# Optimization experiments

Measured on AMD Instinct MI355X. Metric: run time of the kernel, lower is better.

## Reference

```python
import jax, jax.numpy as jnp
import numpy as np
from jax import lax

B = 8192          # batched independent VAD frames (original module is batch=1 streaming)
CUTOFF = 129      # STFT_CUTOFF
STRIDE = 128      # STFT_STRIDE
NFFT = 256        # STFT kernel length (inferred: pad 576->640, stride 128 -> 4 frames)
H = 128           # LSTM hidden size


def conv1d(x, w, b=None, stride=1, padding=0):
    # x: [B, Cin, T], w: [Cout, Cin, K]
    y = lax.conv_general_dilated(x, w, (stride,), [(padding, padding)],
                                 dimension_numbers=("NCH", "OIH", "NCH"))
    if b is not None:
        y = y + b[None, :, None]
    return y


def setup_inputs() -> dict:
    key = jax.random.key(0)
    ks = jax.random.split(key, 40)
    f32 = jnp.float32

    def rn(i, shape, scale=0.1):
        return jax.random.normal(ks[i], shape, dtype=f32) * scale

    inp = {
        "audio": jax.random.normal(ks[0], (B, 576), dtype=f32),
        "h": jnp.zeros((B, H), dtype=f32),
        "c": jnp.zeros((B, H), dtype=f32),
        # STFT basis: 129 real + 129 imag cosine/sine rows, kernel 256
        "forward_basis": rn(1, (2 * CUTOFF, 1, NFFT), 0.1),
        # encoder: 4 conv1d+relu blocks (Silero v5 layout)
        "enc_w1": rn(2, (128, 129, 3)), "enc_b1": rn(3, (128,)),
        "enc_w2": rn(4, (64, 128, 3)), "enc_b2": rn(5, (64,)),
        "enc_w3": rn(6, (64, 64, 3)),  "enc_b3": rn(7, (64,)),
        "enc_w4": rn(8, (128, 64, 3)), "enc_b4": rn(9, (128,)),
        # LSTM cell weights
        "wi": rn(10, (H, H)), "wf": rn(11, (H, H)), "wg": rn(12, (H, H)), "wo": rn(13, (H, H)),
        "ui": rn(14, (H, H)), "uf": rn(15, (H, H)), "ug": rn(16, (H, H)), "uo": rn(17, (H, H)),
        "bxi": rn(18, (H,)), "bxf": rn(19, (H,)), "bxg": rn(20, (H,)), "bxo": rn(21, (H,)),
        "bhi": rn(22, (H,)), "bhf": rn(23, (H,)), "bhg": rn(24, (H,)), "bho": rn(25, (H,)),
        # output head: conv1d 128 -> 1, kernel 1
        "conv_w": rn(26, (1, H, 1)), "conv_b": rn(27, (1,)),
    }
    return inp


def reference(audio, h, c, forward_basis,
              enc_w1, enc_b1, enc_w2, enc_b2, enc_w3, enc_b3, enc_w4, enc_b4,
              wi, wf, wg, wo, ui, uf, ug, uo,
              bxi, bxf, bxg, bxo, bhi, bhf, bhg, bho,
              conv_w, conv_b):
    # STFT via strided conv1d on reflect-padded audio
    x = jnp.pad(audio, ((0, 0), (0, 64)), mode="reflect")[:, None, :]   # [B,1,640]
    x = conv1d(x, forward_basis, stride=STRIDE)                          # [B,258,4]
    real, imag = x[:, :CUTOFF, :], x[:, CUTOFF:, :]
    mag = jnp.sqrt(real ** 2 + imag ** 2)                                # [B,129,4]

    # encoder: conv+relu stack, T: 4 -> 4 -> 2 -> 1 -> 1
    e = jax.nn.relu(conv1d(mag, enc_w1, enc_b1, stride=1, padding=1))
    e = jax.nn.relu(conv1d(e, enc_w2, enc_b2, stride=2, padding=1))
    e = jax.nn.relu(conv1d(e, enc_w3, enc_b3, stride=2, padding=1))
    e = jax.nn.relu(conv1d(e, enc_w4, enc_b4, stride=1, padding=1))
    x = e[:, :, 0]                                                       # [B,128]

    lin = lambda v, W, b: v @ W.T + b
    i_gate = jax.nn.sigmoid(lin(x, wi, bxi) + lin(h, ui, bhi))
    f_gate = jax.nn.sigmoid(lin(x, wf, bxf) + lin(h, uf, bhf))
    g_gate = jnp.tanh(lin(x, wg, bxg) + lin(h, ug, bhg))
    o_gate = jax.nn.sigmoid(lin(x, wo, bxo) + lin(h, uo, bho))
    c_out = f_gate * c + i_gate * g_gate
    h_out = o_gate * jnp.tanh(c_out)

    # output head: relu -> conv1d(128->1, k=1) -> sigmoid -> mean over T(=1)
    y = jax.nn.relu(h_out)                                               # [B,128]
    logit = y @ conv_w[0, :, 0] + conv_b[0]                              # [B]
    prob = jax.nn.sigmoid(logit)[:, None]                                # [B,1]
    return prob, h_out, c_out
```

## Files before the change

### kernel.cpp

```cpp
#include <hip/hip_runtime.h>
#include <math.h>

#define BATCH 8192
typedef unsigned short u16;
typedef unsigned int u32;
typedef __attribute__((ext_vector_type(8))) short bf16x8;
typedef __attribute__((ext_vector_type(4))) float f32x4;
typedef __attribute__((ext_vector_type(4))) unsigned short u16x4;

__device__ __forceinline__ float sigm(float v) { return 1.0f / (1.0f + __expf(-v)); }
__device__ __forceinline__ u16 f2bf(float f) {
    union { float f; u32 u; } v; v.f = f;
    u32 r = v.u + 0x7FFFu + ((v.u >> 16) & 1u);
    return (u16)(r >> 16);
}
__device__ __forceinline__ float bf2f(u16 h) {
    union { u32 u; float f; } v; v.u = ((u32)h) << 16; return v.f;
}
__device__ __forceinline__ void split_store4(float4 v, u16* hp, u16* lp) {
    u16 h0 = f2bf(v.x), h1 = f2bf(v.y), h2 = f2bf(v.z), h3 = f2bf(v.w);
    u16x4 hv = {h0, h1, h2, h3};
    u16x4 lv = {f2bf(v.x - bf2f(h0)), f2bf(v.y - bf2f(h1)),
                f2bf(v.z - bf2f(h2)), f2bf(v.w - bf2f(h3))};
    *(u16x4*)hp = hv; *(u16x4*)lp = lv;
}
__device__ __forceinline__ bf16x8 bfrag(const u16* Bf, int nt, int ch, int nch, int lane) {
    return *(const bf16x8*)(Bf + (((size_t)nt * nch + ch) * 64 + lane) * 8);
}
#define MFMA(a, b, c) __builtin_amdgcn_mfma_f32_16x16x32_bf16(a, b, c, 0, 0, 0)

#define S_FBT 69632
#define S_B1  61440
#define S_B2A 16384
#define S_B2B 24576
#define S_B3  8192
#define S_B4  8192
#define S_BL  131072
#define P_FBT 0
#define P_B1  139264
#define P_B2A 262144
#define P_B2B 294912
#define P_B3  344064
#define P_B4  360448
#define P_BL  376832
#define WEND  638976
#define N_PREP 319488

__global__ __launch_bounds__(256) void k_prep(const float* __restrict__ fb,
                                              const float* __restrict__ w1, const float* __restrict__ w2,
                                              const float* __restrict__ w3, const float* __restrict__ w4,
                                              const float* __restrict__ wi, const float* __restrict__ wf,
                                              const float* __restrict__ wg, const float* __restrict__ wo,
                                              const float* __restrict__ ui, const float* __restrict__ uf,
                                              const float* __restrict__ ug, const float* __restrict__ uo,
                                              u16* __restrict__ wsu) {
    const float* Ws[8] = {wi, wf, wg, wo, ui, uf, ug, uo};
    for (int i = blockIdx.x * 256 + threadIdx.x; i < N_PREP; i += gridDim.x * 256) {
        int r = i;
        float v; int P, S, idx;
        if (r < S_FBT) {
            int f = r >> 9, lane = (r & 511) >> 3, e = r & 7;
            int n = (f >> 3) * 16 + (lane & 15), k = (f & 7) * 32 + (lane >> 4) * 8 + e;
            int c = n >> 1, part = n & 1;
            v = (n < 258) ? fb[(size_t)(c + part * 129) * 256 + k] : 0.f;
            P = P_FBT; S = S_FBT; idx = r;
        } else if ((r -= S_FBT) < S_B1) {
            int kk = r / 20480, r2 = r - kk * 20480;
            int f = r2 >> 9, lane = (r2 & 511) >> 3, e = r2 & 7;
            int n = (f / 5) * 16 + (lane & 15), k = (f % 5) * 32 + (lane >> 4) * 8 + e;
            v = (k < 129) ? w1[(size_t)n * 387 + k * 3 + kk] : 0.f;
            P = P_B1; S = S_B1; idx = r;
        } else if ((r -= S_B1) < S_B2A) {
            int f = r >> 9, lane = (r & 511) >> 3, e = r & 7;
            int n = (f >> 3) * 16 + (lane & 15), k = (f & 7) * 32 + (lane >> 4) * 8 + e;
            v = w2[(size_t)n * 384 + (k & 127) * 3 + (k >> 7) + 1];
            P = P_B2A; S = S_B2A; idx = r;
        } else if ((r -= S_B2A) < S_B2B) {
            int f = r >> 9, lane = (r & 511) >> 3, e = r & 7;
            int n = (f / 12) * 16 + (lane & 15), k = (f % 12) * 32 + (lane >> 4) * 8 + e;
            v = w2[(size_t)n * 384 + (k & 127) * 3 + (k >> 7)];
            P = P_B2B; S = S_B2B; idx = r;
        } else if ((r -= S_B2B) < S_B3) {
            int f = r >> 9, lane = (r & 511) >> 3, e = r & 7;
            int n = (f >> 2) * 16 + (lane & 15), k = (f & 3) * 32 + (lane >> 4) * 8 + e;
            v = w3[(size_t)n * 192 + (k & 63) * 3 + (k >> 6) + 1];
            P = P_B3; S = S_B3; idx = r;
        } else if ((r -= S_B3) < S_B4) {
            int f = r >> 9, lane = (r & 511) >> 3, e = r & 7;
            int n = (f >> 1) * 16 + (lane & 15), k = (f & 1) * 32 + (lane >> 4) * 8 + e;
            v = w4[(size_t)n * 192 + k * 3 + 1];
            P = P_B4; S = S_B4; idx = r;
        } else {
            r -= S_B4;
            int f = r >> 9, lane = (r & 511) >> 3, e = r & 7;
            int n = (f >> 3) * 16 + (lane & 15), k = (f & 7) * 32 + (lane >> 4) * 8 + e;
            int g = n >> 7, j = n & 127;
            v = Ws[g + ((k >= 128) ? 4 : 0)][(size_t)j * 128 + (k & 127)];
            P = P_BL; S = S_BL; idx = r;
        }
        u16 h = f2bf(v);
        wsu[P + idx] = h;
        wsu[P + S + idx] = f2bf(v - bf2f(h));
    }
}

__global__ __launch_bounds__(512) void k_fused1(const float* __restrict__ audio,
                                                const u16* __restrict__ wsu,
                                                const float* __restrict__ b1,
                                                u16* __restrict__ E1H, u16* __restrict__ E1L) {
    __shared__ __align__(16) u16 uni[32256];
    u16* aAh = uni;
    u16* aAl = uni + 11520;
    u16* mAh = uni;
    u16* mAl = uni + 16128;
    const int tid = threadIdx.x;
    const int b0 = blockIdx.x << 4;
    for (int i = tid; i < 16 * 160; i += 512) {
        int bb = i / 160, j4 = (i - bb * 160) * 4;
        const float* ap = audio + (size_t)(b0 + bb) * 576;
        float4 v;
        if (j4 < 576) v = *(const float4*)(ap + j4);
        else { v.x = ap[1150 - j4]; v.y = ap[1149 - j4]; v.z = ap[1148 - j4]; v.w = ap[1147 - j4]; }
        int phys = bb * 720 + j4 + (j4 >> 7) * 8;
        split_store4(v, aAh + phys, aAl + phys);
    }
    __syncthreads();
    const int lane = tid & 63, w = tid >> 6;
    const int m = lane & 15, quad = lane >> 4;
    const u16* fbT = wsu + P_FBT;
    const int tcnt = (w == 7) ? 3 : 2;
    f32x4 acc[4][3];
    #pragma unroll
    for (int mt = 0; mt < 4; ++mt)
        #pragma unroll
        for (int t = 0; t < 3; ++t) acc[mt][t] = (f32x4){0.f, 0.f, 0.f, 0.f};
    for (int ch = 0; ch < 8; ++ch) {
        bf16x8 ah[4], al[4];
        #pragma unroll
        for (int mt = 0; mt < 4; ++mt) {
            int Rm = mt * 16 + m;
            int phys = (Rm >> 2) * 720 + (Rm & 3) * 136 + ch * 32 + quad * 8 + ((ch >= 4) ? 8 : 0);
            ah[mt] = *(const bf16x8*)(aAh + phys);
            al[mt] = *(const bf16x8*)(aAl + phys);
        }
        #pragma unroll
        for (int tt = 0; tt < 3; ++tt) {
            if (tt < tcnt) {
                int t = w * 2 + tt;
                bf16x8 bh = bfrag(fbT, t, ch, 8, lane);
                bf16x8 bl_ = bfrag(fbT + S_FBT, t, ch, 8, lane);
                #pragma unroll
                for (int mt = 0; mt < 4; ++mt) {
                    acc[mt][tt] = MFMA(ah[mt], bh, acc[mt][tt]);
                    acc[mt][tt] = MFMA(ah[mt], bl_, acc[mt][tt]);
                    acc[mt][tt] = MFMA(al[mt], bh, acc[mt][tt]);
                }
            }
        }
    }
    __syncthreads();
    for (int i = tid; i < 16128; i += 512) ((u32*)uni)[i] = 0u;
    __syncthreads();
    #pragma unroll
    for (int tt = 0; tt < 3; ++tt) {
        if (tt < tcnt) {
            int n = (w * 2 + tt) * 16 + m;
            #pragma unroll
            for (int mt = 0; mt < 4; ++mt)
                #pragma unroll
                for (int r = 0; r < 4; ++r) {
                    float vv = acc[mt][tt][r];
                    float s = vv * vv;
                    s += __shfl_xor(s, 1);
                    if (!(n & 1)) {
                        int R = mt * 16 + quad * 4 + r;
                        int bb = R >> 2, t = R & 3, c = n >> 1;
                        float sv = sqrtf(s);
                        u16 h = f2bf(sv);
                        int phys = (bb * 6 + t + 1) * 168 + c;
                        mAh[phys] = h;
                        mAl[phys] = f2bf(sv - bf2f(h));
                    }
                }
        }
    }
    __syncthreads();
    const u16* B1h = wsu + P_B1;
    const u16* B1l = wsu + P_B1 + S_B1;
    f32x4 acc2[4];
    #pragma unroll
    for (int mt = 0; mt < 4; ++mt) acc2[mt] = (f32x4){0.f, 0.f, 0.f, 0.f};
    for (int kk = 0; kk < 3; ++kk) {
        for (int ch = 0; ch < 5; ++ch) {
            bf16x8 bh = bfrag(B1h + kk * 20480, w, ch, 5, lane);
            bf16x8 bl_ = bfrag(B1l + kk * 20480, w, ch, 5, lane);
            #pragma unroll
            for (int mt = 0; mt < 4; ++mt) {
                int Rm = mt * 16 + m;
                int phys = ((Rm >> 2) * 6 + (Rm & 3) + kk) * 168 + ch * 32 + quad * 8;
                bf16x8 ah = *(const bf16x8*)(mAh + phys);
                bf16x8 al = *(const bf16x8*)(mAl + phys);
                acc2[mt] = MFMA(ah, bh, acc2[mt]);
                acc2[mt] = MFMA(ah, bl_, acc2[mt]);
                acc2[mt] = MFMA(al, bh, acc2[mt]);
            }
        }
    }
    {
        int n = w * 16 + m;
        float bv = b1[n];
        #pragma unroll
        for (int mt = 0; mt < 4; ++mt)
            #pragma unroll
            for (int r = 0; r < 4; ++r) {
                int R = mt * 16 + quad * 4 + r;
                float vv = fmaxf(acc2[mt][r] + bv, 0.f);
                u16 h = f2bf(vv);
                size_t idx = (size_t)(b0 + (R >> 2)) * 512 + (R & 3) * 128 + n;
                E1H[idx] = h;
                E1L[idx] = f2bf(vv - bf2f(h));
            }
    }
}

__global__ __launch_bounds__(512) void k_fused2(const u16* __restrict__ E1H, const u16* __restrict__ E1L,
                                                const float* __restrict__ hin,
                                                const u16* __restrict__ wsu,
                                                const float* __restrict__ cin,
                                                const float* __restrict__ b2, const float* __restrict__ b3,
                                                const float* __restrict__ b4,
                                                const float* __restrict__ bxi, const float* __restrict__ bxf,
                                                const float* __restrict__ bxg, const float* __restrict__ bxo,
                                                const float* __restrict__ bhi, const float* __restrict__ bhf,
                                                const float* __restrict__ bhg, const float* __restrict__ bho,
                                                const float* __restrict__ cw, const float* __restrict__ cb,
                                                float* __restrict__ out) {
    __shared__ __align__(16) u16 eAh[16 * 520];
    __shared__ __align__(16) u16 eAl[16 * 520];
    __shared__ __align__(16) u16 s2h[16 * 136];
    __shared__ __align__(16) u16 s2l[16 * 136];
    __shared__ __align__(16) u16 s3h[16 * 72];
    __shared__ __align__(16) u16 s3l[16 * 72];
    __shared__ __align__(16) u16 xhh[16 * 264];
    __shared__ __align__(16) u16 xhl[16 * 264];
    __shared__ float pr[8][16];
    const int tid = threadIdx.x;
    const int b0 = blockIdx.x << 4;
    for (int i = tid; i < 16 * 64; i += 512) {
        int row = i >> 6, c8 = (i & 63) * 8;
        *(uint4*)(eAh + row * 520 + c8) = *(const uint4*)(E1H + (size_t)(b0 + row) * 512 + c8);
        *(uint4*)(eAl + row * 520 + c8) = *(const uint4*)(E1L + (size_t)(b0 + row) * 512 + c8);
    }
    for (int i = tid; i < 16 * 32; i += 512) {
        int row = i >> 5, c4 = (i & 31) * 4;
        float4 v = *(const float4*)(hin + (size_t)(b0 + row) * 128 + c4);
        split_store4(v, xhh + row * 264 + 128 + c4, xhl + row * 264 + 128 + c4);
    }
    __syncthreads();
    const int lane = tid & 63, w = tid >> 6;
    const int m = lane & 15, quad = lane >> 4;
    {
        const int isB = w >> 2, nt = w & 3;
        const int awoff = isB ? 128 : 0;
        const int nch = isB ? 12 : 8;
        const u16* Bh = wsu + (isB ? P_B2B : P_B2A);
        const u16* Bl = Bh + (isB ? S_B2B : S_B2A);
        f32x4 acc = (f32x4){0.f, 0.f, 0.f, 0.f};
        for (int ch = 0; ch < nch; ++ch) {
            int phys = m * 520 + awoff + ch * 32 + quad * 8;
            bf16x8 ah = *(const bf16x8*)(eAh + phys);
            bf16x8 al = *(const bf16x8*)(eAl + phys);
            bf16x8 bh = bfrag(Bh, nt, ch, nch, lane);
            bf16x8 bl_ = bfrag(Bl, nt, ch, nch, lane);
            acc = MFMA(ah, bh, acc);
            acc = MFMA(ah, bl_, acc);
            acc = MFMA(al, bh, acc);
        }
        const int oc = nt * 16 + m;
        const float bv = b2[oc];
        const int col = isB * 64 + oc;
        #pragma unroll
        for (int r = 0; r < 4; ++r) {
            int row = quad * 4 + r;
            float vv = fmaxf(acc[r] + bv, 0.f);
            u16 h = f2bf(vv);
            s2h[row * 136 + col] = h;
            s2l[row * 136 + col] = f2bf(vv - bf2f(h));
        }
    }
    __syncthreads();
    if (w < 4) {
        const u16* Bh = wsu + P_B3;
        const u16* Bl = Bh + S_B3;
        f32x4 acc = (f32x4){0.f, 0.f, 0.f, 0.f};
        for (int ch = 0; ch < 4; ++ch) {
            int phys = m * 136 + ch * 32 + quad * 8;
            bf16x8 ah = *(const bf16x8*)(s2h + phys);
            bf16x8 al = *(const bf16x8*)(s2l + phys);
            bf16x8 bh = bfrag(Bh, w, ch, 4, lane);
            bf16x8 bl_ = bfrag(Bl, w, ch, 4, lane);
            acc = MFMA(ah, bh, acc);
            acc = MFMA(ah, bl_, acc);
            acc = MFMA(al, bh, acc);
        }
        const int n = w * 16 + m;
        const float bv = b3[n];
        #pragma unroll
        for (int r = 0; r < 4; ++r) {
            int row = quad * 4 + r;
            float vv = fmaxf(acc[r] + bv, 0.f);
            u16 h = f2bf(vv);
            s3h[row * 72 + n] = h;
            s3l[row * 72 + n] = f2bf(vv - bf2f(h));
        }
    }
    __syncthreads();
    {
        const u16* Bh = wsu + P_B4;
        const u16* Bl = Bh + S_B4;
        f32x4 acc = (f32x4){0.f, 0.f, 0.f, 0.f};
        for (int ch = 0; ch < 2; ++ch) {
            int phys = m * 72 + ch * 32 + quad * 8;
            bf16x8 ah = *(const bf16x8*)(s3h + phys);
            bf16x8 al = *(const bf16x8*)(s3l + phys);
            bf16x8 bh = bfrag(Bh, w, ch, 2, lane);
            bf16x8 bl_ = bfrag(Bl, w, ch, 2, lane);
            acc = MFMA(ah, bh, acc);
            acc = MFMA(ah, bl_, acc);
            acc = MFMA(al, bh, acc);
        }
        const int n = w * 16 + m;
        const float bv = b4[n];
        #pragma unroll
        for (int r = 0; r < 4; ++r) {
            int row = quad * 4 + r;
            float vv = fmaxf(acc[r] + bv, 0.f);
            u16 h = f2bf(vv);
            xhh[row * 264 + n] = h;
            xhl[row * 264 + n] = f2bf(vv - bf2f(h));
        }
    }
    __syncthreads();
    {
        const u16* BLh = wsu + P_BL;
        const u16* BLl = BLh + S_BL;
        f32x4 acc[4];
        #pragma unroll
        for (int g = 0; g < 4; ++g) acc[g] = (f32x4){0.f, 0.f, 0.f, 0.f};
        for (int ch = 0; ch < 8; ++ch) {
            int phys = m * 264 + ch * 32 + quad * 8;
            bf16x8 ah = *(const bf16x8*)(xhh + phys);
            bf16x8 al = *(const bf16x8*)(xhl + phys);
            #pragma unroll
            for (int g = 0; g < 4; ++g) {
                int nt = g * 8 + w;
                bf16x8 bh = bfrag(BLh, nt, ch, 8, lane);
                bf16x8 bl_ = bfrag(BLl, nt, ch, 8, lane);
                acc[g] = MFMA(ah, bh, acc[g]);
                acc[g] = MFMA(ah, bl_, acc[g]);
                acc[g] = MFMA(al, bh, acc[g]);
            }
        }
        float partial[4];
        const int j = w * 16 + m;
        const float bi = bxi[j] + bhi[j];
        const float bff = bxf[j] + bhf[j];
        const float bgg = bxg[j] + bhg[j];
        const float boo = bxo[j] + bho[j];
        const float cwj = cw[j];
        #pragma unroll
        for (int r = 0; r < 4; ++r) {
            const int b = b0 + quad * 4 + r;
            const float ig = sigm(acc[0][r] + bi);
            const float fg = sigm(acc[1][r] + bff);
            const float gg = tanhf(acc[2][r] + bgg);
            const float og = sigm(acc[3][r] + boo);
            const float ci = cin[(size_t)b * 128 + j];
            const float co = fg * ci + ig * gg;
            const float ho = og * tanhf(co);
            out[(size_t)BATCH + (size_t)b * 128 + j] = ho;
            out[(size_t)BATCH + (size_t)BATCH * 128 + (size_t)b * 128 + j] = co;
            partial[r] = fmaxf(ho, 0.f) * cwj;
        }
        #pragma unroll
        for (int off = 1; off < 16; off <<= 1)
            #pragma unroll
            for (int r = 0; r < 4; ++r) partial[r] += __shfl_xor(partial[r], off);
        if (m == 0) {
            #pragma unroll
            for (int r = 0; r < 4; ++r) pr[w][quad * 4 + r] = partial[r];
        }
    }
    __syncthreads();
    if (tid < 16) {
        float s = cb[0];
        #pragma unroll
        for (int g = 0; g < 8; ++g) s += pr[g][tid];
        out[b0 + tid] = sigm(s);
    }
}

extern "C" void kernel_launch(void* const* d_in, const int* in_sizes, int n_in,
                              void* d_out, int out_size, void* d_ws, size_t ws_size,
                              hipStream_t stream) {
    const float* audio = (const float*)d_in[0];
    const float* hin   = (const float*)d_in[1];
    const float* cin   = (const float*)d_in[2];
    const float* fb    = (const float*)d_in[3];
    const float* w1    = (const float*)d_in[4];
    const float* b1    = (const float*)d_in[5];
    const float* w2    = (const float*)d_in[6];
    const float* b2    = (const float*)d_in[7];
    const float* w3    = (const float*)d_in[8];
    const float* b3    = (const float*)d_in[9];
    const float* w4    = (const float*)d_in[10];
    const float* b4    = (const float*)d_in[11];
    const float* wi    = (const float*)d_in[12];
    const float* wf    = (const float*)d_in[13];
    const float* wg    = (const float*)d_in[14];
    const float* wo    = (const float*)d_in[15];
    const float* ui    = (const float*)d_in[16];
    const float* uf    = (const float*)d_in[17];
    const float* ug    = (const float*)d_in[18];
    const float* uo    = (const float*)d_in[19];
    const float* bxi   = (const float*)d_in[20];
    const float* bxf   = (const float*)d_in[21];
    const float* bxg   = (const float*)d_in[22];
    const float* bxo   = (const float*)d_in[23];
    const float* bhi   = (const float*)d_in[24];
    const float* bhf   = (const float*)d_in[25];
    const float* bhg   = (const float*)d_in[26];
    const float* bho   = (const float*)d_in[27];
    const float* cw    = (const float*)d_in[28];
    const float* cb    = (const float*)d_in[29];
    float* out = (float*)d_out;

    u16* wsu = (u16*)d_ws;
    u16* E1H = wsu + WEND;
    u16* E1L = E1H + (size_t)BATCH * 512;

    k_prep<<<640, 256, 0, stream>>>(fb, w1, w2, w3, w4, wi, wf, wg, wo, ui, uf, ug, uo, wsu);
    k_fused1<<<BATCH / 16, 512, 0, stream>>>(audio, wsu, b1, E1H, E1L);
    k_fused2<<<BATCH / 16, 512, 0, stream>>>(E1H, E1L, hin, wsu, cin, b2, b3, b4,
                                             bxi, bxf, bxg, bxo, bhi, bhf, bhg, bho,
                                             cw, cb, out);
}
```

Before: 181.4 us.

## Fuse first and second stage kernels into one, keeping encoder activations in LDS

Merges k_fused1 and k_fused2 into a single kernel that keeps the conv1 output (hi/lo bf16 split) in shared memory instead of writing it to global workspace and reading it back. The shared buffer is reused for the later encoder and LSTM stages, with an added barrier. This removes a kernel launch and roughly 16 MB of global traffic. The cost is higher register pressure and a larger single kernel, which may lower occupancy. An unroll-2 pragma is also added on the LSTM channel loop.

```diff
diff --git a/kernel.cpp b/kernel.cpp
--- a/kernel.cpp
+++ b/kernel.cpp
@@ -43,7 +43,6 @@
 #define P_B3  344064
 #define P_B4  360448
 #define P_BL  376832
-#define WEND  638976
 #define N_PREP 319488
 
 __global__ __launch_bounds__(256) void k_prep(const float* __restrict__ fb,
@@ -104,15 +103,31 @@
     }
 }
 
-__global__ __launch_bounds__(512) void k_fused1(const float* __restrict__ audio,
-                                                const u16* __restrict__ wsu,
-                                                const float* __restrict__ b1,
-                                                u16* __restrict__ E1H, u16* __restrict__ E1L) {
+__global__ __launch_bounds__(512) void k_all(const float* __restrict__ audio,
+                                             const u16* __restrict__ wsu,
+                                             const float* __restrict__ hin, const float* __restrict__ cin,
+                                             const float* __restrict__ b1, const float* __restrict__ b2,
+                                             const float* __restrict__ b3, const float* __restrict__ b4,
+                                             const float* __restrict__ bxi, const float* __restrict__ bxf,
+                                             const float* __restrict__ bxg, const float* __restrict__ bxo,
+                                             const float* __restrict__ bhi, const float* __restrict__ bhf,
+                                             const float* __restrict__ bhg, const float* __restrict__ bho,
+                                             const float* __restrict__ cw, const float* __restrict__ cb,
+                                             float* __restrict__ out) {
     __shared__ __align__(16) u16 uni[32256];
     u16* aAh = uni;
     u16* aAl = uni + 11520;
     u16* mAh = uni;
     u16* mAl = uni + 16128;
+    u16* eAh = uni;
+    u16* eAl = uni + 8320;
+    u16* s2h = uni + 16640;
+    u16* s2l = uni + 18816;
+    u16* s3h = uni + 20992;
+    u16* s3l = uni + 22144;
+    u16* xhh = uni + 23296;
+    u16* xhl = uni + 27520;
+    float* pr = (float*)(uni + 31744);
     const int tid = threadIdx.x;
     const int b0 = blockIdx.x << 4;
     for (int i = tid; i < 16 * 160; i += 512) {
@@ -206,6 +221,7 @@
             }
         }
     }
+    __syncthreads();
     {
         int n = w * 16 + m;
         float bv = b1[n];
@@ -216,40 +232,10 @@
                 int R = mt * 16 + quad * 4 + r;
                 float vv = fmaxf(acc2[mt][r] + bv, 0.f);
                 u16 h = f2bf(vv);
-                size_t idx = (size_t)(b0 + (R >> 2)) * 512 + (R & 3) * 128 + n;
-                E1H[idx] = h;
-                E1L[idx] = f2bf(vv - bf2f(h));
+                int phys = (R >> 2) * 520 + (R & 3) * 128 + n;
+                eAh[phys] = h;
+                eAl[phys] = f2bf(vv - bf2f(h));
             }
-    }
-}
-
-__global__ __launch_bounds__(512) void k_fused2(const u16* __restrict__ E1H, const u16* __restrict__ E1L,
-                                                const float* __restrict__ hin,
-                                                const u16* __restrict__ wsu,
-                                                const float* __restrict__ cin,
-                                                const float* __restrict__ b2, const float* __restrict__ b3,
-                                                const float* __restrict__ b4,
-                                                const float* __restrict__ bxi, const float* __restrict__ bxf,
-                                                const float* __restrict__ bxg, const float* __restrict__ bxo,
-                                                const float* __restrict__ bhi, const float* __restrict__ bhf,
-                                                const float* __restrict__ bhg, const float* __restrict__ bho,
-                                                const float* __restrict__ cw, const float* __restrict__ cb,
-                                                float* __restrict__ out) {
-    __shared__ __align__(16) u16 eAh[16 * 520];
-    __shared__ __align__(16) u16 eAl[16 * 520];
-    __shared__ __align__(16) u16 s2h[16 * 136];
-    __shared__ __align__(16) u16 s2l[16 * 136];
-    __shared__ __align__(16) u16 s3h[16 * 72];
-    __shared__ __align__(16) u16 s3l[16 * 72];
-    __shared__ __align__(16) u16 xhh[16 * 264];
-    __shared__ __align__(16) u16 xhl[16 * 264];
-    __shared__ float pr[8][16];
-    const int tid = threadIdx.x;
-    const int b0 = blockIdx.x << 4;
-    for (int i = tid; i < 16 * 64; i += 512) {
-        int row = i >> 6, c8 = (i & 63) * 8;
-        *(uint4*)(eAh + row * 520 + c8) = *(const uint4*)(E1H + (size_t)(b0 + row) * 512 + c8);
-        *(uint4*)(eAl + row * 520 + c8) = *(const uint4*)(E1L + (size_t)(b0 + row) * 512 + c8);
     }
     for (int i = tid; i < 16 * 32; i += 512) {
         int row = i >> 5, c4 = (i & 31) * 4;
@@ -257,24 +243,22 @@
         split_store4(v, xhh + row * 264 + 128 + c4, xhl + row * 264 + 128 + c4);
     }
     __syncthreads();
-    const int lane = tid & 63, w = tid >> 6;
-    const int m = lane & 15, quad = lane >> 4;
     {
         const int isB = w >> 2, nt = w & 3;
         const int awoff = isB ? 128 : 0;
         const int nch = isB ? 12 : 8;
         const u16* Bh = wsu + (isB ? P_B2B : P_B2A);
         const u16* Bl = Bh + (isB ? S_B2B : S_B2A);
-        f32x4 acc = (f32x4){0.f, 0.f, 0.f, 0.f};
+        f32x4 a2 = (f32x4){0.f, 0.f, 0.f, 0.f};
         for (int ch = 0; ch < nch; ++ch) {
             int phys = m * 520 + awoff + ch * 32 + quad * 8;
             bf16x8 ah = *(const bf16x8*)(eAh + phys);
             bf16x8 al = *(const bf16x8*)(eAl + phys);
             bf16x8 bh = bfrag(Bh, nt, ch, nch, lane);
             bf16x8 bl_ = bfrag(Bl, nt, ch, nch, lane);
-            acc = MFMA(ah, bh, acc);
-            acc = MFMA(ah, bl_, acc);
-            acc = MFMA(al, bh, acc);
+            a2 = MFMA(ah, bh, a2);
+            a2 = MFMA(ah, bl_, a2);
+            a2 = MFMA(al, bh, a2);
         }
         const int oc = nt * 16 + m;
         const float bv = b2[oc];
@@ -282,7 +266,7 @@
         #pragma unroll
         for (int r = 0; r < 4; ++r) {
             int row = quad * 4 + r;
-            float vv = fmaxf(acc[r] + bv, 0.f);
+            float vv = fmaxf(a2[r] + bv, 0.f);
             u16 h = f2bf(vv);
             s2h[row * 136 + col] = h;
             s2l[row * 136 + col] = f2bf(vv - bf2f(h));
@@ -292,23 +276,23 @@
     if (w < 4) {
         const u16* Bh = wsu + P_B3;
         const u16* Bl = Bh + S_B3;
-        f32x4 acc = (f32x4){0.f, 0.f, 0.f, 0.f};
+        f32x4 a3 = (f32x4){0.f, 0.f, 0.f, 0.f};
         for (int ch = 0; ch < 4; ++ch) {
             int phys = m * 136 + ch * 32 + quad * 8;
             bf16x8 ah = *(const bf16x8*)(s2h + phys);
             bf16x8 al = *(const bf16x8*)(s2l + phys);
             bf16x8 bh = bfrag(Bh, w, ch, 4, lane);
             bf16x8 bl_ = bfrag(Bl, w, ch, 4, lane);
-            acc = MFMA(ah, bh, acc);
-            acc = MFMA(ah, bl_, acc);
-            acc = MFMA(al, bh, acc);
+            a3 = MFMA(ah, bh, a3);
+            a3 = MFMA(ah, bl_, a3);
+            a3 = MFMA(al, bh, a3);
         }
         const int n = w * 16 + m;
         const float bv = b3[n];
         #pragma unroll
         for (int r = 0; r < 4; ++r) {
             int row = quad * 4 + r;
-            float vv = fmaxf(acc[r] + bv, 0.f);
+            float vv = fmaxf(a3[r] + bv, 0.f);
             u16 h = f2bf(vv);
             s3h[row * 72 + n] = h;
             s3l[row * 72 + n] = f2bf(vv - bf2f(h));
@@ -318,23 +302,23 @@
     {
         const u16* Bh = wsu + P_B4;
         const u16* Bl = Bh + S_B4;
-        f32x4 acc = (f32x4){0.f, 0.f, 0.f, 0.f};
+        f32x4 a4 = (f32x4){0.f, 0.f, 0.f, 0.f};
         for (int ch = 0; ch < 2; ++ch) {
             int phys = m * 72 + ch * 32 + quad * 8;
             bf16x8 ah = *(const bf16x8*)(s3h + phys);
             bf16x8 al = *(const bf16x8*)(s3l + phys);
             bf16x8 bh = bfrag(Bh, w, ch, 2, lane);
             bf16x8 bl_ = bfrag(Bl, w, ch, 2, lane);
-            acc = MFMA(ah, bh, acc);
-            acc = MFMA(ah, bl_, acc);
-            acc = MFMA(al, bh, acc);
+            a4 = MFMA(ah, bh, a4);
+            a4 = MFMA(ah, bl_, a4);
+            a4 = MFMA(al, bh, a4);
         }
         const int n = w * 16 + m;
         const float bv = b4[n];
         #pragma unroll
         for (int r = 0; r < 4; ++r) {
             int row = quad * 4 + r;
-            float vv = fmaxf(acc[r] + bv, 0.f);
+            float vv = fmaxf(a4[r] + bv, 0.f);
             u16 h = f2bf(vv);
             xhh[row * 264 + n] = h;
             xhl[row * 264 + n] = f2bf(vv - bf2f(h));
@@ -344,9 +328,10 @@
     {
         const u16* BLh = wsu + P_BL;
         const u16* BLl = BLh + S_BL;
-        f32x4 acc[4];
-        #pragma unroll
-        for (int g = 0; g < 4; ++g) acc[g] = (f32x4){0.f, 0.f, 0.f, 0.f};
+        f32x4 ag[4];
+        #pragma unroll
+        for (int g = 0; g < 4; ++g) ag[g] = (f32x4){0.f, 0.f, 0.f, 0.f};
+        #pragma unroll 2
         for (int ch = 0; ch < 8; ++ch) {
             int phys = m * 264 + ch * 32 + quad * 8;
             bf16x8 ah = *(const bf16x8*)(xhh + phys);
@@ -356,9 +341,9 @@
                 int nt = g * 8 + w;
                 bf16x8 bh = bfrag(BLh, nt, ch, 8, lane);
                 bf16x8 bl_ = bfrag(BLl, nt, ch, 8, lane);
-                acc[g] = MFMA(ah, bh, acc[g]);
-                acc[g] = MFMA(ah, bl_, acc[g]);
-                acc[g] = MFMA(al, bh, acc[g]);
+                ag[g] = MFMA(ah, bh, ag[g]);
+                ag[g] = MFMA(ah, bl_, ag[g]);
+                ag[g] = MFMA(al, bh, ag[g]);
             }
         }
         float partial[4];
@@ -371,10 +356,10 @@
         #pragma unroll
         for (int r = 0; r < 4; ++r) {
             const int b = b0 + quad * 4 + r;
-            const float ig = sigm(acc[0][r] + bi);
-            const float fg = sigm(acc[1][r] + bff);
-            const float gg = tanhf(acc[2][r] + bgg);
-            const float og = sigm(acc[3][r] + boo);
+            const float ig = sigm(ag[0][r] + bi);
+            const float fg = sigm(ag[1][r] + bff);
+            const float gg = tanhf(ag[2][r] + bgg);
+            const float og = sigm(ag[3][r] + boo);
             const float ci = cin[(size_t)b * 128 + j];
             const float co = fg * ci + ig * gg;
             const float ho = og * tanhf(co);
@@ -388,14 +373,14 @@
             for (int r = 0; r < 4; ++r) partial[r] += __shfl_xor(partial[r], off);
         if (m == 0) {
             #pragma unroll
-            for (int r = 0; r < 4; ++r) pr[w][quad * 4 + r] = partial[r];
+            for (int r = 0; r < 4; ++r) pr[w * 16 + quad * 4 + r] = partial[r];
         }
     }
     __syncthreads();
     if (tid < 16) {
         float s = cb[0];
         #pragma unroll
-        for (int g = 0; g < 8; ++g) s += pr[g][tid];
+        for (int g = 0; g < 8; ++g) s += pr[g * 16 + tid];
         out[b0 + tid] = sigm(s);
     }
 }
@@ -436,12 +421,9 @@
     float* out = (float*)d_out;
 
     u16* wsu = (u16*)d_ws;
-    u16* E1H = wsu + WEND;
-    u16* E1L = E1H + (size_t)BATCH * 512;
 
     k_prep<<<640, 256, 0, stream>>>(fb, w1, w2, w3, w4, wi, wf, wg, wo, ui, uf, ug, uo, wsu);
-    k_fused1<<<BATCH / 16, 512, 0, stream>>>(audio, wsu, b1, E1H, E1L);
-    k_fused2<<<BATCH / 16, 512, 0, stream>>>(E1H, E1L, hin, wsu, cin, b2, b3, b4,
-                                             bxi, bxf, bxg, bxo, bhi, bhf, bhg, bho,
-                                             cw, cb, out);
-}
+    k_all<<<BATCH / 16, 512, 0, stream>>>(audio, wsu, hin, cin, b1, b2, b3, b4,
+                                          bxi, bxf, bxg, bxo, bhi, bhf, bhg, bho,
+                                          cw, cb, out);
+}
```

After: 172.3 us. 5.1% less time.
